# Kernel tuning notes

Measured on AMD Instinct MI355X. Metric: run time of the kernel, lower is better.

## Reference

```python
import jax, jax.numpy as jnp
import numpy as np

B, N_HEADS, H, W, DIM = 8, 12, 32, 32, 768
HEAD_DIM = DIM // N_HEADS  # 64
N = 1 + H * W  # cls token + spatial tokens


def setup_inputs() -> dict:
    key = jax.random.key(0)
    ks = jax.random.split(key, 8)
    x = jax.random.normal(ks[0], (B, N, DIM), dtype=jnp.float32)
    mask = jax.random.bernoulli(ks[1], 0.7, (B, N))
    mask = mask.at[:, 0].set(True)  # cls token always valid
    qkv_w = jax.random.normal(ks[2], (DIM, 3 * DIM), dtype=jnp.float32) * 0.02
    qkv_b = jnp.zeros((3 * DIM,), dtype=jnp.float32)
    proj_w = jax.random.normal(ks[3], (DIM, DIM), dtype=jnp.float32) * 0.02
    proj_b = jnp.zeros((DIM,), dtype=jnp.float32)
    rel_pos_h = jax.random.normal(ks[4], (2 * H - 1, HEAD_DIM), dtype=jnp.float32) * 0.02
    rel_pos_w = jax.random.normal(ks[5], (2 * W - 1, HEAD_DIM), dtype=jnp.float32) * 0.02
    return {"x": x, "mask": mask, "qkv_w": qkv_w, "qkv_b": qkv_b,
            "proj_w": proj_w, "proj_b": proj_b,
            "rel_pos_h": rel_pos_h, "rel_pos_w": rel_pos_w}


def _rel_pos_bias(q_spatial, rel_pos_h, rel_pos_w):
    # q_spatial: [B, heads, H, W, head_dim]; q_shape == k_shape so ratios are 1
    idx_h = jnp.arange(H)[:, None] - jnp.arange(H)[None, :] + (H - 1)  # [H, H]
    idx_w = jnp.arange(W)[:, None] - jnp.arange(W)[None, :] + (W - 1)  # [W, W]
    Rh = rel_pos_h[idx_h]  # [H, kH, c]
    Rw = rel_pos_w[idx_w]  # [W, kW, c]
    rel_h = jnp.einsum('byhwc,hkc->byhwk', q_spatial, Rh)  # [B,heads,H,W,kH]
    rel_w = jnp.einsum('byhwc,wkc->byhwk', q_spatial, Rw)  # [B,heads,H,W,kW]
    bias = rel_h[..., :, None] + rel_w[..., None, :]        # [B,heads,H,W,kH,kW]
    return bias.reshape(q_spatial.shape[0], q_spatial.shape[1], H * W, H * W)


def reference(x, mask, qkv_w, qkv_b, proj_w, proj_b, rel_pos_h, rel_pos_w):
    scale = HEAD_DIM ** -0.5
    qkv = (x @ qkv_w + qkv_b).reshape(B, N, 3, N_HEADS, HEAD_DIM)
    qkv = jnp.transpose(qkv, (2, 0, 3, 1, 4))
    q, k, v = qkv[0], qkv[1], qkv[2]
    attn = jnp.einsum('bhqd,bhkd->bhqk', q, k) * scale  # [B,heads,N,N]
    # spatial relative position bias on the non-cls block (cal_rel_pos_spatial)
    r_q = q[:, :, 1:, :].reshape(B, N_HEADS, H, W, HEAD_DIM)
    bias = _rel_pos_bias(r_q, rel_pos_h, rel_pos_w)
    attn = attn.at[:, :, 1:, 1:].add(bias)
    # attention mask: outer product of 1D token masks
    m = mask.astype(attn.dtype)
    mask2d = jnp.einsum('bi,bj->bij', m, m)[:, None, :, :]
    attn = attn - 1e9 * (1.0 - mask2d)
    attn = jax.nn.softmax(attn, axis=-1)
    out = jnp.einsum('bhqk,bhkd->bhqd', attn, v)
    out = jnp.transpose(out, (0, 2, 1, 3)).reshape(B, N, DIM)
    out = out @ proj_w + proj_b
    # GlobalMaxPoolLayer with use_class_token=True: masked GAP + max over spatial tokens
    x_sp = out[:, 1:, :]
    m_sp = mask[:, 1:].astype(jnp.float32)[..., None]
    avg = jnp.sum(x_sp * m_sp, axis=1, keepdims=True) / (jnp.sum(m_sp, axis=1, keepdims=True) + 1e-7)
    mx = jnp.max(x_sp, axis=1, keepdims=True)
    pooled = jnp.concatenate([avg, mx], axis=-1)  # [B, 1, 2*DIM]
    return pooled
```

## Files before the change

kernel.cpp:

```cpp
#include <hip/hip_runtime.h>
#include <hip/hip_bf16.h>

typedef __attribute__((ext_vector_type(8))) short short8v;
typedef __attribute__((ext_vector_type(4))) float f32x4;
typedef __attribute__((ext_vector_type(16))) float f32x16;

constexpr int B_  = 8;
constexpr int NH  = 12;
constexpr int DIM = 768;
constexpr int HD  = 64;
constexpr int N_  = 1025;
constexpr int NSP = 1024;
constexpr int K3  = 2304;
constexpr int VT  = 34;

constexpr size_t KV_BYTES = (size_t)B_*NH*VT*4096;

constexpr size_t OFF_MASK  = 0;
constexpr size_t OFF_PC    = 49152;
constexpr size_t OFF_QKVWT = 65536;
constexpr size_t OFF_PROJWT= OFF_QKVWT + (size_t)K3*768*2;
constexpr size_t OFF_Q     = OFF_PROJWT + (size_t)768*768*2;
constexpr size_t OFF_K     = OFF_Q + (size_t)B_*NH*N_*HD*2;
constexpr size_t OFF_V     = OFF_K + KV_BYTES;
constexpr size_t OFF_AO    = OFF_V + KV_BYTES;
constexpr size_t OFF_PS    = OFF_AO + (size_t)8192*768*2;
constexpr size_t OFF_PM    = OFF_PS + 64*768*4;
constexpr size_t OFF_XB    = OFF_PM + 64*768*4;

__device__ inline float b2f(unsigned short u) {
  union { unsigned int ui; float f; } x; x.ui = ((unsigned int)u) << 16; return x.f;
}
__device__ inline unsigned short f2b(float f) {
  union { float f; unsigned int u; } x; x.f = f;
  unsigned int r = x.u + 0x7FFFu + ((x.u >> 16) & 1u);
  return (unsigned short)(r >> 16);
}
__device__ inline unsigned int cvtpk(float lo, float hi) {
  unsigned int r;
  asm("v_cvt_pk_bf16_f32 %0, %1, %2" : "=v"(r) : "v"(lo), "v"(hi));
  return r;
}
__device__ inline short8v pack8(float4 lo, float4 hi) {
  union { unsigned int u[4]; short8v s; } r;
  r.u[0] = cvtpk(lo.x, lo.y); r.u[1] = cvtpk(lo.z, lo.w);
  r.u[2] = cvtpk(hi.x, hi.y); r.u[3] = cvtpk(hi.z, hi.w);
  return r.s;
}
__device__ inline float fexp2(float x) {
  float r;
  asm("v_exp_f32 %0, %1" : "=v"(r) : "v"(x));
  return r;
}
__device__ inline void plswap(unsigned int& a, unsigned int& b) {
  asm("v_permlane32_swap_b32 %0, %1" : "+v"(a), "+v"(b));
}
__device__ inline void gload16(const void* g, void* l) {
  __builtin_amdgcn_global_load_lds(
      (const __attribute__((address_space(1))) void*)g,
      (__attribute__((address_space(3))) void*)l, 16, 0, 0);
}
template<int NWG>
__device__ inline int xcd_swz(int bid) {
  constexpr int q = NWG / 8, r = NWG % 8;
  const int x = bid & 7, i = bid >> 3;
  return (x < r ? x * (q + 1) : r * (q + 1) + (x - r) * q) + i;
}

__global__ __launch_bounds__(256) void preproc(
    const unsigned char* __restrict__ mraw, float* __restrict__ mask_f,
    float* __restrict__ pcnt, unsigned short* __restrict__ kW,
    unsigned short* __restrict__ vW,
    const float* __restrict__ qkv_w, const float* __restrict__ proj_w,
    unsigned short* __restrict__ qkvwT, unsigned short* __restrict__ projwT,
    const float* __restrict__ x, unsigned short* __restrict__ xb)
{
  const int g = blockIdx.x, t = threadIdx.x;
  if (g < 96) {
    unsigned short* kz = kW + ((size_t)g * VT + 32) * 2048;
    for (int i = t; i < 2048; i += 256) kz[i] = 0;
    unsigned short* vz = vW + ((size_t)g * VT + 32) * 2048;
    for (int i = t; i < 2048; i += 256) vz[i] = 0;
    unsigned short* xz = xb + (size_t)8200 * 768;
    for (int i = g * 256 + t; i < 120 * 768; i += 96 * 256) xz[i] = 0;
    return;
  }
  if (g == 96) {
    __shared__ int flags[2];
    __shared__ float cnt8[8];
    if (t < 2) flags[t] = 0;
    if (t < 8) cnt8[t] = 0.f;
    __syncthreads();
    const int n = B_ * N_;
    int f1 = 0, f0 = 0;
    for (int i = t; i < n; i += 256) {
      unsigned char vv = mraw[i];
      if (vv) { int m = i & 3; if (m == 1) f1 = 1; if (m == 0) f0 = 1; }
    }
    if (f1) atomicOr(&flags[0], 1);
    if (f0) atomicOr(&flags[1], 1);
    __syncthreads();
    const bool isBool = flags[0] != 0;
    const bool isInt  = !isBool && (flags[1] != 0);
    for (int i = t; i < n; i += 256) {
      float v;
      if (isBool)     v = mraw[i] ? 1.f : 0.f;
      else if (isInt) v = ((const int*)mraw)[i] ? 1.f : 0.f;
      else            v = ((const float*)mraw)[i];
      mask_f[i] = v;
      const int b = i / 1025, nn = i - b * 1025;
      if (nn > 0) atomicAdd(&cnt8[b], v);
    }
    __syncthreads();
    if (t < 8) pcnt[t] = cnt8[t];
    return;
  }
  if (g < 2401) {
    __shared__ float tile[32][33];
    const float* in; unsigned short* out; int N, bx, by;
    if (g < 1825) { const int idx = g - 97;  in = qkv_w;  out = qkvwT;  N = K3;  bx = idx % 72; by = idx / 72; }
    else          { const int idx = g - 1825; in = proj_w; out = projwT; N = 768; bx = idx % 24; by = idx / 24; }
    const int tx = t & 31, ty0 = t >> 5;
    const int n0 = bx * 32, k0 = by * 32;
#pragma unroll
    for (int i = 0; i < 4; ++i) {
      const int r = ty0 + i * 8;
      tile[r][tx] = in[(size_t)(k0 + r) * N + n0 + tx];
    }
    __syncthreads();
#pragma unroll
    for (int i = 0; i < 4; ++i) {
      const int r = ty0 + i * 8;
      out[(size_t)(n0 + r) * 768 + k0 + tx] = f2b(tile[tx][r]);
    }
    return;
  }
  const int idx = g - 2401;
  const int n4 = 8200 * 768 / 4;
  for (int i = idx * 256 + t; i < n4; i += 2048 * 256) {
    float4 v = *(const float4*)&x[i * 4];
    ushort4 u;
    u.x = f2b(v.x); u.y = f2b(v.y); u.z = f2b(v.z); u.w = f2b(v.w);
    *(ushort4*)&xb[i * 4] = u;
  }
}

template<int MODE, int GX, int NWG>
__global__ __launch_bounds__(256) void gemm_bf16(
    const unsigned short* __restrict__ A, const unsigned short* __restrict__ BT,
    const float* __restrict__ bias,
    unsigned short* __restrict__ qo, unsigned short* __restrict__ ko,
    unsigned short* __restrict__ vo,
    const float* __restrict__ mask_f, float* __restrict__ psum,
    float* __restrict__ pmax, int M)
{
  __shared__ unsigned short As[2][128 * 32];
  __shared__ unsigned short Bs[2][128 * 32];
  __shared__ float Ms[128];
  const int t = threadIdx.x;
  const int l = t & 63, w = t >> 6;
  const int lg16 = l >> 4, lm16 = l & 15;
  const int wr = w >> 1, wc = w & 1;
  const int wg = xcd_swz<NWG>(blockIdx.x);
  const int by = wg / GX, bx = wg - by * GX;
  const int m0 = by * 128, n0 = bx * 128;

  if (MODE == 1 && t < 128) {
    const int b0 = m0 >> 10, nr = m0 & 1023;
    Ms[t] = mask_f[b0 * N_ + 1 + nr + t];
  }

  f32x4 acc[4][4];
#pragma unroll
  for (int i = 0; i < 4; ++i)
#pragma unroll
    for (int j = 0; j < 4; ++j) acc[i][j] = (f32x4){0.f, 0.f, 0.f, 0.f};

  const int row0 = t >> 2, qq = (t & 3) * 8;
  const unsigned short* Asrc0 = A + (size_t)(m0 + row0) * 768 + qq;
  const unsigned short* Asrc1 = A + (size_t)(m0 + row0 + 64) * 768 + qq;
  const unsigned short* Bsrc0 = BT + (size_t)(n0 + row0) * 768 + qq;
  const unsigned short* Bsrc1 = BT + (size_t)(n0 + row0 + 64) * 768 + qq;

#define STAGE(bi, k0)                                                    \
  do {                                                                   \
    gload16(Asrc0 + (k0), (char*)&As[bi][0] + w * 1024);                 \
    gload16(Asrc1 + (k0), (char*)&As[bi][0] + 4096 + w * 1024);          \
    gload16(Bsrc0 + (k0), (char*)&Bs[bi][0] + w * 1024);                 \
    gload16(Bsrc1 + (k0), (char*)&Bs[bi][0] + 4096 + w * 1024);          \
  } while (0)

  STAGE(0, 0);

#pragma unroll
  for (int kk = 0; kk < 24; ++kk) {
    const int cur = kk & 1;
    if (kk < 23) {
      STAGE(cur ^ 1, (kk + 1) * 32);
      asm volatile("s_waitcnt vmcnt(4)" ::: "memory");
    } else {
      asm volatile("s_waitcnt vmcnt(0)" ::: "memory");
    }
    asm volatile("s_barrier" ::: "memory");
    short8v af[4], bf4[4];
#pragma unroll
    for (int mi = 0; mi < 4; ++mi)
      af[mi] = *(const short8v*)&As[cur][(wr * 64 + mi * 16 + lm16) * 32 + lg16 * 8];
#pragma unroll
    for (int ni = 0; ni < 4; ++ni)
      bf4[ni] = *(const short8v*)&Bs[cur][(wc * 64 + ni * 16 + lm16) * 32 + lg16 * 8];
#pragma unroll
    for (int mi = 0; mi < 4; ++mi)
#pragma unroll
      for (int ni = 0; ni < 4; ++ni)
        acc[mi][ni] = __builtin_amdgcn_mfma_f32_16x16x32_bf16(
            af[mi], bf4[ni], acc[mi][ni], 0, 0, 0);
    asm volatile("s_barrier" ::: "memory");
  }
#undef STAGE

  if (MODE == 1) {
    __syncthreads();
    float* sred = (float*)&As[0][0];
    float* xred = sred + 256;
#pragma unroll
    for (int ni = 0; ni < 4; ++ni) {
      const int cidx = wc * 64 + ni * 16 + lm16;
      const float bv = bias[n0 + cidx];
      float s = 0.f, xm = -3.402823466e+38f;
#pragma unroll
      for (int mi = 0; mi < 4; ++mi)
#pragma unroll
        for (int r = 0; r < 4; ++r) {
          const float v = acc[mi][ni][r] + bv;
          const float m = Ms[wr * 64 + mi * 16 + lg16 * 4 + r];
          s = fmaf(v, m, s);
          xm = fmaxf(xm, v);
        }
      s += __shfl_xor(s, 16);
      s += __shfl_xor(s, 32);
      xm = fmaxf(xm, __shfl_xor(xm, 16));
      xm = fmaxf(xm, __shfl_xor(xm, 32));
      if (lg16 == 0) {
        sred[wr * 128 + cidx] = s;
        xred[wr * 128 + cidx] = xm;
      }
    }
    __syncthreads();
    if (t < 128) {
      const float s  = sred[t] + sred[128 + t];
      const float xm = fmaxf(xred[t], xred[128 + t]);
      psum[(size_t)by * 768 + n0 + t] = s;
      pmax[(size_t)by * 768 + n0 + t] = xm;
    }
  } else {
#pragma unroll
    for (int mi = 0; mi < 4; ++mi) {
      const int r0 = m0 + wr * 64 + mi * 16 + lg16 * 4;
      const int b0d = r0 / 1025;
      const int n0d = r0 - b0d * 1025;
#pragma unroll
      for (int ni = 0; ni < 4; ++ni) {
        const int col = n0 + wc * 64 + ni * 16 + lm16;
        const int which = col / 768;
        const int rem = col - which * 768;
        const int head = rem >> 6, d = rem & 63;
        const float bv = bias[col];
#pragma unroll
        for (int r = 0; r < 4; ++r) {
          const int grow = r0 + r;
          if (grow >= M) continue;
          int b = b0d, n = n0d + r;
          if (n >= 1025) { b += 1; n -= 1025; }
          const unsigned short val = f2b(acc[mi][ni][r] + bv);
          const int bh = b * NH + head;
          if (which == 0) {
            qo[((size_t)bh * N_ + n) * HD + d] = val;
          } else if (which == 1) {
            ko[((size_t)bh * VT + (n >> 5)) * 2048 + (d >> 4) * 512 +
               ((((d >> 3) & 1) << 5) + (n & 31)) * 8 + (d & 7)] = val;
          } else {
            const int kvloc = n & 31;
            vo[((size_t)bh * VT + (n >> 5)) * 2048 +
               ((d >> 5) * 2 + (kvloc >> 4)) * 512 +
               ((((kvloc >> 3) & 1) << 5) + (d & 31)) * 8 + (kvloc & 7)] = val;
          }
        }
      }
    }
  }
}

__global__ __launch_bounds__(256, 3) void attn_mfma(
    const unsigned short* __restrict__ qp, const unsigned short* __restrict__ kp,
    const unsigned short* __restrict__ vp, const float* __restrict__ mask_f,
    const float* __restrict__ rph, const float* __restrict__ rpw,
    unsigned short* __restrict__ ao)
{
  const int bid = blockIdx.x;
  const int xcd = bid & 7, wx = bid >> 3;
  const int qblk = wx / 12, hl = wx - qblk * 12;
  const int bh = xcd * 12 + hl;
  const int b = bh / NH, head = bh - b * NH;

  const int t = threadIdx.x, w = t >> 6, lane = t & 63;
  const int qi = lane & 31, h = lane >> 5;
  const int row = w * 32 + qi;
  constexpr float L2E = 1.44269504f;
  constexpr float SCL = 0.125f * L2E;
  constexpr float MCOL = -1.44269504e9f;
  constexpr float THR_L = 2.885f;

  __shared__ __align__(16) float bh_lds[128][34];
  __shared__ __align__(16) float ct_lds[1088];
  __shared__ __align__(16) unsigned short T16[128][64];
  float* ctm = (float*)&T16[0][0];

  const unsigned short* qbp = qp + (size_t)bh * N_ * HD;
  const unsigned short* kbp = kp + (size_t)bh * VT * 2048;
  const unsigned short* vbp = vp + (size_t)bh * VT * 2048;
  const int qw0 = qblk * 128 + w * 32;
  const int q = qw0 + qi;

  for (int i = t; i < 1088; i += 256)
    ct_lds[i] = (i < N_) ? (MCOL * (1.f - mask_f[b * N_ + i])) : -2e30f;

  short8v qf[4];
#pragma unroll
  for (int c = 0; c < 4; ++c)
    qf[c] = *(const short8v*)&qbp[(size_t)(1 + q) * HD + c * 16 + h * 8];

  {
    const int hq = q >> 5;
    f32x16 sbh = {}, sb1 = {}, sb2 = {};
    const float* rh0 = rph + (size_t)(hq + 31 - qi) * HD + h * 8;
    const float* rw1 = rpw + (size_t)qi * HD + h * 8;
    const float* rw2 = rpw + (size_t)(qi < 31 ? 32 + qi : 62) * HD + h * 8;
#pragma unroll
    for (int c = 0; c < 4; ++c) {
      short8v a1 = pack8(*(const float4*)(rh0 + c * 16), *(const float4*)(rh0 + c * 16 + 4));
      sbh = __builtin_amdgcn_mfma_f32_32x32x16_bf16(a1, qf[c], sbh, 0, 0, 0);
      short8v a2 = pack8(*(const float4*)(rw1 + c * 16), *(const float4*)(rw1 + c * 16 + 4));
      sb1 = __builtin_amdgcn_mfma_f32_32x32x16_bf16(a2, qf[c], sb1, 0, 0, 0);
      short8v a3 = pack8(*(const float4*)(rw2 + c * 16), *(const float4*)(rw2 + c * 16 + 4));
      sb2 = __builtin_amdgcn_mfma_f32_32x32x16_bf16(a3, qf[c], sb2, 0, 0, 0);
    }
#pragma unroll
    for (int r = 0; r < 16; ++r) {
      const int kh = (r & 3) + 8 * (r >> 2) + 4 * h;
      bh_lds[row][kh]   = sbh[r] * L2E;
      T16[row][kh]      = f2b(sb1[r] * L2E);
      T16[row][kh + 32] = f2b(sb2[r] * L2E);
    }
    if (h == 0) { bh_lds[row][32] = 0.f; bh_lds[row][33] = 0.f; }
  }
  __syncthreads();

  float bwv[16];
#pragma unroll
  for (int r = 0; r < 16; ++r) {
    const int kvS = (r & 3) + 8 * (r >> 2) + 4 * h;
    const int kw = (kvS + 31) & 31;
    bwv[r] = b2f(T16[row][qi - kw + 31]);
  }
  __syncthreads();
  for (int i = t; i < 1088; i += 256)
    ctm[i] = (i <= 1024) ? MCOL : -2e30f;
  __syncthreads();

  const float mi_s = mask_f[b * N_ + 1 + q];
  const bool mzero = (mi_s == 0.f);
  const float* ctp = mzero ? ctm : ct_lds;
  const float h0sel = (h == 0) ? 1.f : 0.f;
  float m_lm = -1e30f, l_lane = 0.f;
  float bh_prev = -bwv[0];
  f32x16 oaccA = {}, oaccB = {};

  const char* kptr = (const char*)kbp + lane * 16;
  const char* vptr = (const char*)vbp + lane * 16;

  short8v kf[4];
#pragma unroll
  for (int c = 0; c < 4; ++c) kf[c] = *(const short8v*)(kptr + c * 1024);
  kptr += 4096;
  f32x16 sP = {}, sQ = {};
  sP = __builtin_amdgcn_mfma_f32_32x32x16_bf16(kf[0], qf[0], sP, 0, 0, 0);
  sP = __builtin_amdgcn_mfma_f32_32x32x16_bf16(kf[1], qf[1], sP, 0, 0, 0);
  sP = __builtin_amdgcn_mfma_f32_32x32x16_bf16(kf[2], qf[2], sP, 0, 0, 0);
  sP = __builtin_amdgcn_mfma_f32_32x32x16_bf16(kf[3], qf[3], sP, 0, 0, 0);

#define AITER(KT, SC, SN, DOPREF)                                            \
  do {                                                                       \
    short8v vf00 = *(const short8v*)(vptr);                                  \
    short8v vf01 = *(const short8v*)(vptr + 1024);                           \
    short8v vf10 = *(const short8v*)(vptr + 2048);                           \
    short8v vf11 = *(const short8v*)(vptr + 3072);                           \
    vptr += 4096;                                                            \
    if (DOPREF) {                                                            \
      kf[0] = *(const short8v*)(kptr);                                       \
      kf[1] = *(const short8v*)(kptr + 1024);                                \
      kf[2] = *(const short8v*)(kptr + 2048);                                \
      kf[3] = *(const short8v*)(kptr + 3072);                                \
      kptr += 4096;                                                          \
    }                                                                        \
    const float bh_k = bh_lds[row][KT];                                      \
    const float bh_use = mzero ? 0.f : bh_k;                                 \
    f32x4 ct4[4];                                                            \
    ct4[0] = *(const f32x4*)&ctp[(KT) * 32 + h * 4];                         \
    ct4[1] = *(const f32x4*)&ctp[(KT) * 32 + 8 + h * 4];                     \
    ct4[2] = *(const f32x4*)&ctp[(KT) * 32 + 16 + h * 4];                    \
    ct4[3] = *(const f32x4*)&ctp[(KT) * 32 + 24 + h * 4];                    \
    float lgp[16];                                                           \
    _Pragma("unroll")                                                        \
    for (int r = 0; r < 16; ++r)                                             \
      lgp[r] = fmaf(SCL, SC[r], bwv[r] + ct4[r >> 2][r & 3]);                \
    lgp[0] = fmaf(h0sel, bh_prev - bh_use, lgp[0]);                          \
    bh_prev = bh_k;                                                          \
    float a0 = fmaxf(lgp[0], lgp[1]),  a1 = fmaxf(lgp[2], lgp[3]);           \
    float a2 = fmaxf(lgp[4], lgp[5]),  a3 = fmaxf(lgp[6], lgp[7]);           \
    float a4 = fmaxf(lgp[8], lgp[9]),  a5 = fmaxf(lgp[10], lgp[11]);         \
    float a6 = fmaxf(lgp[12], lgp[13]), a7 = fmaxf(lgp[14], lgp[15]);        \
    float tm = fmaxf(fmaxf(fmaxf(a0, a1), fmaxf(a2, a3)),                    \
                     fmaxf(fmaxf(a4, a5), fmaxf(a6, a7)));                   \
    tm = fmaxf(tm, __shfl_xor(tm, 32));                                      \
    const float tmT = tm + bh_use;                                           \
    if (__any(tmT > m_lm + THR_L)) {                                         \
      const float nm = fmaxf(m_lm, tmT);                                     \
      const float rf = fexp2(m_lm - nm);                                     \
      m_lm = nm; l_lane *= rf;                                               \
      _Pragma("unroll")                                                      \
      for (int r = 0; r < 16; ++r) { oaccA[r] *= rf; oaccB[r] *= rf; }       \
    }                                                                        \
    const float mm = bh_use - m_lm;                                          \
    float p[16];                                                             \
    _Pragma("unroll")                                                        \
    for (int r = 0; r < 16; ++r) p[r] = fexp2(lgp[r] + mm);                  \
    l_lane += (((p[0]+p[1])+(p[2]+p[3]))+((p[4]+p[5])+(p[6]+p[7])))          \
            + (((p[8]+p[9])+(p[10]+p[11]))+((p[12]+p[13])+(p[14]+p[15])));   \
    unsigned int x0 = cvtpk(p[0], p[1]),  x1 = cvtpk(p[2], p[3]);            \
    unsigned int z0 = cvtpk(p[4], p[5]),  z1 = cvtpk(p[6], p[7]);            \
    plswap(x0, z0); plswap(x1, z1);                                          \
    unsigned int y0 = cvtpk(p[8], p[9]),  y1 = cvtpk(p[10], p[11]);          \
    unsigned int w0_ = cvtpk(p[12], p[13]), w1_ = cvtpk(p[14], p[15]);       \
    plswap(y0, w0_); plswap(y1, w1_);                                        \
    union { unsigned int u[4]; short8v v; } uf1, uf2;                        \
    uf1.u[0] = x0; uf1.u[1] = x1; uf1.u[2] = z0; uf1.u[3] = z1;              \
    uf2.u[0] = y0; uf2.u[1] = y1; uf2.u[2] = w0_; uf2.u[3] = w1_;            \
    if (DOPREF) {                                                            \
      f32x16 sn = {};                                                        \
      sn = __builtin_amdgcn_mfma_f32_32x32x16_bf16(kf[0], qf[0], sn, 0, 0, 0); \
      sn = __builtin_amdgcn_mfma_f32_32x32x16_bf16(kf[1], qf[1], sn, 0, 0, 0); \
      sn = __builtin_amdgcn_mfma_f32_32x32x16_bf16(kf[2], qf[2], sn, 0, 0, 0); \
      sn = __builtin_amdgcn_mfma_f32_32x32x16_bf16(kf[3], qf[3], sn, 0, 0, 0); \
      SN = sn;                                                               \
    }                                                                        \
    oaccA = __builtin_amdgcn_mfma_f32_32x32x16_bf16(vf00, uf1.v, oaccA, 0, 0, 0); \
    oaccA = __builtin_amdgcn_mfma_f32_32x32x16_bf16(vf01, uf2.v, oaccA, 0, 0, 0); \
    oaccB = __builtin_amdgcn_mfma_f32_32x32x16_bf16(vf10, uf1.v, oaccB, 0, 0, 0); \
    oaccB = __builtin_amdgcn_mfma_f32_32x32x16_bf16(vf11, uf2.v, oaccB, 0, 0, 0); \
  } while (0)

  for (int kt2 = 0; kt2 < 16; ++kt2) {
    AITER(2 * kt2,     sP, sQ, true);
    AITER(2 * kt2 + 1, sQ, sP, true);
  }
  AITER(32, sP, sQ, false);
#undef AITER

  __syncthreads();

  const float l_tot = l_lane + __shfl_xor(l_lane, 32);
  const float inv = 1.f / l_tot;
  char* tbase = (char*)&T16[0][0] + row * 128;
  const int rsw = (row & 7) << 4;
#pragma unroll
  for (int r = 0; r < 16; r += 2) {
    const int d = (r & 3) + 8 * (r >> 2) + 4 * h;
    const unsigned int uA = cvtpk(oaccA[r] * inv, oaccA[r + 1] * inv);
    const unsigned int uB = cvtpk(oaccB[r] * inv, oaccB[r + 1] * inv);
    const int bo1 = 2 * d, bo2 = 2 * d + 64;
    *(unsigned int*)(tbase + (((bo1 & ~15) ^ rsw) | (bo1 & 15))) = uA;
    *(unsigned int*)(tbase + (((bo2 & ~15) ^ rsw) | (bo2 & 15))) = uB;
  }
  const int q2 = lane >> 1, hb = lane & 1;
  const int srow = w * 32 + q2;
  const char* sbase = (const char*)&T16[0][0] + srow * 128;
  const int ssw = srow & 7;
  unsigned short* dst =
      ao + (size_t)(b * NSP + qw0 + q2) * DIM + head * HD + hb * 32;
#pragma unroll
  for (int i = 0; i < 4; ++i) {
    const int ci = hb * 4 + i;
    short8v v = *(const short8v*)(sbase + ((ci ^ ssw) << 4));
    *(short8v*)(dst + i * 8) = v;
  }
}

__global__ __launch_bounds__(256) void pool_stage2(
    const float* __restrict__ psum, const float* __restrict__ pmax,
    const float* __restrict__ pcnt, float* __restrict__ out)
{
  const int b = blockIdx.y;
  const int c = blockIdx.x * 256 + threadIdx.x;
  float s = 0.f, mx = -3.402823466e+38f;
#pragma unroll
  for (int z = 0; z < 8; ++z) {
    s  += psum[(size_t)(b * 8 + z) * 768 + c];
    mx  = fmaxf(mx, pmax[(size_t)(b * 8 + z) * 768 + c]);
  }
  const float cnt = pcnt[b];
  out[b * 1536 + c]       = s / (cnt + 1e-7f);
  out[b * 1536 + 768 + c] = mx;
}

extern "C" void kernel_launch(void* const* d_in, const int* in_sizes, int n_in,
                              void* d_out, int out_size, void* d_ws, size_t ws_size,
                              hipStream_t stream) {
  const float* x      = (const float*)d_in[0];
  const unsigned char* mraw = (const unsigned char*)d_in[1];
  const float* qkv_w  = (const float*)d_in[2];
  const float* qkv_b  = (const float*)d_in[3];
  const float* proj_w = (const float*)d_in[4];
  const float* proj_b = (const float*)d_in[5];
  const float* rph    = (const float*)d_in[6];
  const float* rpw    = (const float*)d_in[7];

  char* ws = (char*)d_ws;
  float*          mask_f = (float*)(ws + OFF_MASK);
  float*          pcnt   = (float*)(ws + OFF_PC);
  unsigned short* qkvwT  = (unsigned short*)(ws + OFF_QKVWT);
  unsigned short* projwT = (unsigned short*)(ws + OFF_PROJWT);
  unsigned short* qW     = (unsigned short*)(ws + OFF_Q);
  unsigned short* kW     = (unsigned short*)(ws + OFF_K);
  unsigned short* vW     = (unsigned short*)(ws + OFF_V);
  unsigned short* aoW    = (unsigned short*)(ws + OFF_AO);
  float*          psum   = (float*)(ws + OFF_PS);
  float*          pmax   = (float*)(ws + OFF_PM);
  unsigned short* xb     = (unsigned short*)(ws + OFF_XB);

  preproc<<<4449, 256, 0, stream>>>(mraw, mask_f, pcnt, kW, vW,
                                    qkv_w, proj_w, qkvwT, projwT, x, xb);

  gemm_bf16<0, 18, 1170><<<1170, 256, 0, stream>>>(
      xb, qkvwT, qkv_b, qW, kW, vW, nullptr, nullptr, nullptr, 8200);

  attn_mfma<<<768, 256, 0, stream>>>(qW, kW, vW, mask_f, rph, rpw, aoW);

  gemm_bf16<1, 6, 384><<<384, 256, 0, stream>>>(
      aoW, projwT, proj_b, nullptr, nullptr, nullptr,
      mask_f, psum, pmax, 8192);

  pool_stage2<<<dim3(3, B_), 256, 0, stream>>>(psum, pmax, pcnt, (float*)d_out);
}
```

Measured before the change: 161.4 us.

## Double K-tile depth to 64 with XOR-swizzled LDS layout in bf16 GEMM

The GEMM main loop now stages 64-wide K slices per iteration instead of 32, halving the number of barrier pairs and outer iterations. The shared-memory layout is XOR-swizzled by row so the 16-byte fragment reads avoid bank conflicts. The mask staging in shared memory is dropped and the epilogue reads mask values straight from global memory. The trade-off is twice the LDS footprint (64 KB), which may lower occupancy, plus redundant global mask loads in the epilogue.

```diff
diff --git a/kernel.cpp b/kernel.cpp
--- a/kernel.cpp
+++ b/kernel.cpp
@@ -154,9 +154,8 @@
     const float* __restrict__ mask_f, float* __restrict__ psum,
     float* __restrict__ pmax, int M)
 {
-  __shared__ unsigned short As[2][128 * 32];
-  __shared__ unsigned short Bs[2][128 * 32];
-  __shared__ float Ms[128];
+  __shared__ unsigned short As[2][128 * 64];
+  __shared__ unsigned short Bs[2][128 * 64];
   const int t = threadIdx.x;
   const int l = t & 63, w = t >> 6;
   const int lg16 = l >> 4, lm16 = l & 15;
@@ -165,56 +164,67 @@
   const int by = wg / GX, bx = wg - by * GX;
   const int m0 = by * 128, n0 = bx * 128;
 
-  if (MODE == 1 && t < 128) {
-    const int b0 = m0 >> 10, nr = m0 & 1023;
-    Ms[t] = mask_f[b0 * N_ + 1 + nr + t];
-  }
-
   f32x4 acc[4][4];
 #pragma unroll
   for (int i = 0; i < 4; ++i)
 #pragma unroll
     for (int j = 0; j < 4; ++j) acc[i][j] = (f32x4){0.f, 0.f, 0.f, 0.f};
 
-  const int row0 = t >> 2, qq = (t & 3) * 8;
-  const unsigned short* Asrc0 = A + (size_t)(m0 + row0) * 768 + qq;
-  const unsigned short* Asrc1 = A + (size_t)(m0 + row0 + 64) * 768 + qq;
-  const unsigned short* Bsrc0 = BT + (size_t)(n0 + row0) * 768 + qq;
-  const unsigned short* Bsrc1 = BT + (size_t)(n0 + row0 + 64) * 768 + qq;
-
-#define STAGE(bi, k0)                                                    \
-  do {                                                                   \
-    gload16(Asrc0 + (k0), (char*)&As[bi][0] + w * 1024);                 \
-    gload16(Asrc1 + (k0), (char*)&As[bi][0] + 4096 + w * 1024);          \
-    gload16(Bsrc0 + (k0), (char*)&Bs[bi][0] + w * 1024);                 \
-    gload16(Bsrc1 + (k0), (char*)&Bs[bi][0] + 4096 + w * 1024);          \
+  const int srow = t >> 3;
+  const int scol = ((t & 7) ^ (srow & 7)) * 8;
+  const unsigned short* Asrc0 = A + (size_t)(m0 + srow) * 768 + scol;
+  const unsigned short* Bsrc0 = BT + (size_t)(n0 + srow) * 768 + scol;
+  char* const Adst = (char*)&As[0][0] + w * 1024;
+  char* const Bdst = (char*)&Bs[0][0] + w * 1024;
+  constexpr int RS = 32 * 768;
+  constexpr int BUF = 128 * 64 * 2;
+
+#define STAGE(bi, k0)                                                     \
+  do {                                                                    \
+    gload16(Asrc0 + (k0),          Adst + (bi) * BUF);                    \
+    gload16(Asrc0 + (k0) + RS,     Adst + (bi) * BUF + 4096);             \
+    gload16(Asrc0 + (k0) + 2 * RS, Adst + (bi) * BUF + 8192);             \
+    gload16(Asrc0 + (k0) + 3 * RS, Adst + (bi) * BUF + 12288);            \
+    gload16(Bsrc0 + (k0),          Bdst + (bi) * BUF);                    \
+    gload16(Bsrc0 + (k0) + RS,     Bdst + (bi) * BUF + 4096);             \
+    gload16(Bsrc0 + (k0) + 2 * RS, Bdst + (bi) * BUF + 8192);             \
+    gload16(Bsrc0 + (k0) + 3 * RS, Bdst + (bi) * BUF + 12288);            \
   } while (0)
 
   STAGE(0, 0);
 
 #pragma unroll
-  for (int kk = 0; kk < 24; ++kk) {
+  for (int kk = 0; kk < 12; ++kk) {
     const int cur = kk & 1;
-    if (kk < 23) {
-      STAGE(cur ^ 1, (kk + 1) * 32);
-      asm volatile("s_waitcnt vmcnt(4)" ::: "memory");
+    if (kk < 11) {
+      STAGE(cur ^ 1, (kk + 1) * 64);
+      asm volatile("s_waitcnt vmcnt(8)" ::: "memory");
     } else {
       asm volatile("s_waitcnt vmcnt(0)" ::: "memory");
     }
     asm volatile("s_barrier" ::: "memory");
-    short8v af[4], bf4[4];
-#pragma unroll
-    for (int mi = 0; mi < 4; ++mi)
-      af[mi] = *(const short8v*)&As[cur][(wr * 64 + mi * 16 + lm16) * 32 + lg16 * 8];
-#pragma unroll
-    for (int ni = 0; ni < 4; ++ni)
-      bf4[ni] = *(const short8v*)&Bs[cur][(wc * 64 + ni * 16 + lm16) * 32 + lg16 * 8];
-#pragma unroll
-    for (int mi = 0; mi < 4; ++mi)
-#pragma unroll
-      for (int ni = 0; ni < 4; ++ni)
-        acc[mi][ni] = __builtin_amdgcn_mfma_f32_16x16x32_bf16(
-            af[mi], bf4[ni], acc[mi][ni], 0, 0, 0);
+#pragma unroll
+    for (int ksub = 0; ksub < 2; ++ksub) {
+      short8v af[4], bf4[4];
+#pragma unroll
+      for (int mi = 0; mi < 4; ++mi) {
+        const int R = wr * 64 + mi * 16 + lm16;
+        af[mi] = *(const short8v*)
+            &As[cur][R * 64 + (((ksub * 4 + lg16) ^ (R & 7)) * 8)];
+      }
+#pragma unroll
+      for (int ni = 0; ni < 4; ++ni) {
+        const int R = wc * 64 + ni * 16 + lm16;
+        bf4[ni] = *(const short8v*)
+            &Bs[cur][R * 64 + (((ksub * 4 + lg16) ^ (R & 7)) * 8)];
+      }
+#pragma unroll
+      for (int mi = 0; mi < 4; ++mi)
+#pragma unroll
+        for (int ni = 0; ni < 4; ++ni)
+          acc[mi][ni] = __builtin_amdgcn_mfma_f32_16x16x32_bf16(
+              af[mi], bf4[ni], acc[mi][ni], 0, 0, 0);
+    }
     asm volatile("s_barrier" ::: "memory");
   }
 #undef STAGE
@@ -223,6 +233,7 @@
     __syncthreads();
     float* sred = (float*)&As[0][0];
     float* xred = sred + 256;
+    const int b0 = m0 >> 10, nr = m0 & 1023;
 #pragma unroll
     for (int ni = 0; ni < 4; ++ni) {
       const int cidx = wc * 64 + ni * 16 + lm16;
@@ -233,7 +244,8 @@
 #pragma unroll
         for (int r = 0; r < 4; ++r) {
           const float v = acc[mi][ni][r] + bv;
-          const float m = Ms[wr * 64 + mi * 16 + lg16 * 4 + r];
+          const float m =
+              mask_f[b0 * N_ + 1 + nr + wr * 64 + mi * 16 + lg16 * 4 + r];
           s = fmaf(v, m, s);
           xm = fmaxf(xm, v);
         }
```

Measured after the change: 169.8 us. 5.2% more time.
